# Performance work log

Hardware: AMD Instinct MI355X
Metric: run time of the kernel (lower is better)

The kernel has to match this reference:

```python
import jax, jax.numpy as jnp
import numpy as np

N_NODES = 50000
N_EDGES = 600000
N_GRAPHS = 256
D = 128          # hidden_dim
L = 4            # num_layer
OUT = 1          # output_dim
ATOM_DIMS = [119, 5, 12, 12, 10, 6, 6, 2, 2]   # table size = dim+1, pad to 120
BOND_DIMS = [6, 6, 2, 2, 2]                    # table size = dim+1, pad to 7
BN_EPS = 1e-5


def setup_inputs() -> dict:
    key = jax.random.key(0)
    ks = jax.random.split(key, 16)
    x = jax.random.randint(ks[0], (N_NODES, 9), 0, 3)
    edge_index = jax.random.randint(ks[1], (2, N_EDGES), 0, N_NODES)
    edge_attr = jax.random.randint(ks[2], (N_EDGES, 5), 0, 3)
    batch = jnp.sort(jax.random.randint(ks[3], (N_NODES,), 0, N_GRAPHS))
    s = 0.1
    # padded atom embedding tables: [9, 120, D] (rows beyond dim+1 unused)
    atom_emb = jax.random.normal(ks[4], (9, 120, D), jnp.float32) * s
    # padded bond tables per layer: [L, 5, 7, D]
    bond_emb = jax.random.normal(ks[5], (L, 5, 7, D), jnp.float32) * s
    lin_w = jax.random.normal(ks[6], (L, D, D), jnp.float32) * (1.0 / np.sqrt(D))
    lin_b = jnp.zeros((L, D), jnp.float32)
    bn_gamma = jnp.ones((L, D), jnp.float32)
    bn_beta = jnp.zeros((L, D), jnp.float32)
    mlp_w1 = jax.random.normal(ks[7], (D // 2, D), jnp.float32) * (1.0 / np.sqrt(D))
    mlp_b1 = jnp.zeros((D // 2,), jnp.float32)
    mlp_w2 = jax.random.normal(ks[8], (OUT, D // 2), jnp.float32) * (1.0 / np.sqrt(D // 2))
    mlp_b2 = jnp.zeros((OUT,), jnp.float32)
    return dict(x=x, edge_index=edge_index, edge_attr=edge_attr, batch=batch,
                atom_emb=atom_emb, bond_emb=bond_emb, lin_w=lin_w, lin_b=lin_b,
                bn_gamma=bn_gamma, bn_beta=bn_beta,
                mlp_w1=mlp_w1, mlp_b1=mlp_b1, mlp_w2=mlp_w2, mlp_b2=mlp_b2)


def _multi_embed(tables, idx):
    # tables: [F, V, D], idx: [N, F] -> sum_f tables[f][idx[:, f]]
    return jax.vmap(lambda t, i: t[i], in_axes=(0, 1))(tables, idx).sum(0)


def reference(x, edge_index, edge_attr, batch, atom_emb, bond_emb, lin_w, lin_b,
              bn_gamma, bn_beta, mlp_w1, mlp_b1, mlp_w2, mlp_b2):
    n = x.shape[0]
    loop = jnp.arange(n, dtype=edge_index.dtype)
    src = jnp.concatenate([edge_index[0], loop])           # x_j (source)
    dst = jnp.concatenate([edge_index[1], loop])           # aggregate into target i
    ea = jnp.concatenate([edge_attr, jnp.zeros((n, 5), edge_attr.dtype)], axis=0)
    h = _multi_embed(atom_emb, x)                          # [N, D]
    for l in range(L):
        e_emb = _multi_embed(bond_emb[l], ea)              # [E+N, D]
        msg = h[src] + e_emb                               # gather + add
        aggr = jax.ops.segment_sum(msg, dst, num_segments=n)
        z = aggr @ lin_w[l].T + lin_b[l]
        mu = z.mean(0)
        var = z.var(0)                                     # biased, matches torch BN fwd
        h = jax.nn.relu((z - mu) * jax.lax.rsqrt(var + BN_EPS) * bn_gamma[l] + bn_beta[l])
    # global mean pool
    sums = jax.ops.segment_sum(h, batch, num_segments=N_GRAPHS)
    cnt = jax.ops.segment_sum(jnp.ones((n,), h.dtype), batch, num_segments=N_GRAPHS)
    g = sums / jnp.maximum(cnt, 1.0)[:, None]
    # MLP head (dropout inactive at inference)
    out = jax.nn.relu(g @ mlp_w1.T + mlp_b1) @ mlp_w2.T + mlp_b2
    return out
```

## Files before the change

kernel.cpp:

```cpp
#include <hip/hip_runtime.h>
#include <hip/hip_bf16.h>
#include <stdint.h>

#define D 128
#define NGRAPH 256
#define BN_EPS 1e-5f
#define TAB_ROWS 105
#define TAB_SZ (TAB_ROWS * D)
#define AGG_BLOCKS 512
#define AGG_THREADS 1024
#define MAXDEG 48
#define GW_TS 136

typedef unsigned short u16;
typedef __attribute__((ext_vector_type(8))) short bf16x8;
typedef __attribute__((ext_vector_type(4))) float f32x4;

__device__ inline u16 f2bf(float a) {
  return __builtin_bit_cast(u16, __float2bfloat16(a));
}
__device__ inline uint32_t pk2(float a, float b) {
  return (uint32_t)f2bf(a) | ((uint32_t)f2bf(b) << 16);
}
__device__ inline float bflo(uint32_t u) { return __builtin_bit_cast(float, u << 16); }
__device__ inline float bfhi(uint32_t u) { return __builtin_bit_cast(float, u & 0xffff0000u); }
__device__ inline void unpack8(uint4 v, float* f) {
  f[0] = bflo(v.x); f[1] = bfhi(v.x); f[2] = bflo(v.y); f[3] = bfhi(v.y);
  f[4] = bflo(v.z); f[5] = bfhi(v.z); f[6] = bflo(v.w); f[7] = bfhi(v.w);
}

__global__ __launch_bounds__(256) void setup_kernel(
    const int* __restrict__ x, const float* __restrict__ atom_emb,
    float* __restrict__ h0,
    const int* __restrict__ src, const int* __restrict__ dst,
    const int* __restrict__ attr, int* __restrict__ deg,
    uint2* __restrict__ edges, int ne,
    const int* __restrict__ batch, int* __restrict__ goff,
    float* __restrict__ gsum, int n) {
  int b = blockIdx.x, tid = threadIdx.x;
  int nscat = (ne + 255) >> 8;
  int nemb = (n * 32 + 255) >> 8;
  if (b < nscat) {
    int e = b * 256 + tid;
    if (e >= ne) return;
    int d = dst[e];
    int slot = atomicAdd(&deg[d], 1);
    if (slot >= MAXDEG) return;
    int a0 = attr[e * 5 + 0], a1 = attr[e * 5 + 1], a2 = attr[e * 5 + 2];
    int a3 = attr[e * 5 + 3], a4 = attr[e * 5 + 4];
    uint32_t packed = (uint32_t)(a0 * 7 + a1) | ((uint32_t)(a2 * 7 + a3) << 8) |
                      ((uint32_t)a4 << 16);
    uint2 r; r.x = (uint32_t)src[e]; r.y = packed;
    edges[(size_t)d * MAXDEG + slot] = r;
  } else if (b < nscat + nemb) {
    int t = (b - nscat) * 256 + tid;
    int node = t >> 5, cq = t & 31;
    if (node >= n) return;
    float4 acc = {0.f, 0.f, 0.f, 0.f};
#pragma unroll
    for (int f = 0; f < 9; f++) {
      int idx = x[node * 9 + f];
      const float4* row = (const float4*)(atom_emb + ((size_t)f * 120 + idx) * D);
      float4 v = row[cq];
      acc.x += v.x; acc.y += v.y; acc.z += v.z; acc.w += v.w;
    }
    ((float4*)(h0 + (size_t)node * D))[cq] = acc;
  } else {
    if (b == nscat + nemb) {
      for (int t = tid; t < 4 * 2 * D; t += 256) gsum[t] = 0.f;
    }
    int i = (b - nscat - nemb) * 256 + tid;
    if (i >= n) return;
    int bb = batch[i];
    if (i == 0) {
      for (int g = 0; g <= bb; g++) goff[g] = 0;
    } else {
      int pb = batch[i - 1];
      for (int g = pb + 1; g <= bb; g++) goff[g] = i;
    }
    if (i == n - 1) {
      for (int g = bb + 1; g <= NGRAPH; g++) goff[g] = n;
    }
  }
}

__global__ __launch_bounds__(128) void prep_kernel(
    const float* __restrict__ bemb, const float* __restrict__ linw,
    u16* __restrict__ tabAll) {
  __shared__ float row[D];
  int b = blockIdx.x, c = threadIdx.x;
  int l = b / TAB_ROWS, r = b % TAB_ROWS;
  const float* bond = bemb + (size_t)l * 5 * 7 * D;
  const float* W = linw + (size_t)l * D * D;
  float v;
  if (r < 49)
    v = bond[(0 * 7 + r / 7) * D + c] + bond[(1 * 7 + r % 7) * D + c];
  else if (r < 98) {
    int rr = r - 49;
    v = bond[(2 * 7 + rr / 7) * D + c] + bond[(3 * 7 + rr % 7) * D + c];
  } else
    v = bond[(4 * 7 + (r - 98)) * D + c];
  row[c] = v;
  __syncthreads();
  float s = 0.f;
  for (int k = 0; k < D; k++) s += row[k] * W[(size_t)c * D + k];
  tabAll[((size_t)l * TAB_ROWS + r) * D + c] = f2bf(s);
}

__global__ __launch_bounds__(256) void gemm_kernel(const float* __restrict__ in,
                                                   const float* __restrict__ W,
                                                   const float* __restrict__ gsum,
                                                   const float* __restrict__ gamma,
                                                   const float* __restrict__ beta,
                                                   float invN,
                                                   u16* __restrict__ out, int M) {
  __shared__ u16 wlds[128 * GW_TS];
  __shared__ float bns[2 * D];
  int tid = threadIdx.x;
  for (int i = tid; i < 4096; i += 256) {
    int row = i >> 5, c4 = (i & 31) * 4;
    float4 v = ((const float4*)W)[i];
    uint2 o = {pk2(v.x, v.y), pk2(v.z, v.w)};
    *(uint2*)(wlds + row * GW_TS + c4) = o;
  }
  if (gsum && tid < D) {
    float s = gsum[tid], q = gsum[D + tid];
    float mu = s * invN;
    float var = q * invN - mu * mu;
    float sc = rsqrtf(var + BN_EPS) * gamma[tid];
    bns[tid] = sc;
    bns[D + tid] = beta[tid] - mu * sc;
  }
  __syncthreads();

  int wave = tid >> 6, lane = tid & 63;
  int quad = lane >> 4, l16 = lane & 15;
  int m0 = blockIdx.x * 64 + wave * 16;
  int m = m0 + l16;
  bool valid = m < M;

  f32x4 acc[8];
#pragma unroll
  for (int t = 0; t < 8; t++) acc[t] = (f32x4){0.f, 0.f, 0.f, 0.f};

#pragma unroll
  for (int kk = 0; kk < 4; kk++) {
    int k0 = kk * 32 + quad * 8;
    bf16x8 a;
    if (valid) {
      float4 v0 = *(const float4*)(in + (size_t)m * D + k0);
      float4 v1 = *(const float4*)(in + (size_t)m * D + k0 + 4);
      if (gsum) {
        float4 sc0 = *(const float4*)(bns + k0);
        float4 sc1 = *(const float4*)(bns + k0 + 4);
        float4 sh0 = *(const float4*)(bns + D + k0);
        float4 sh1 = *(const float4*)(bns + D + k0 + 4);
        v0.x = fmaxf(v0.x * sc0.x + sh0.x, 0.f);
        v0.y = fmaxf(v0.y * sc0.y + sh0.y, 0.f);
        v0.z = fmaxf(v0.z * sc0.z + sh0.z, 0.f);
        v0.w = fmaxf(v0.w * sc0.w + sh0.w, 0.f);
        v1.x = fmaxf(v1.x * sc1.x + sh1.x, 0.f);
        v1.y = fmaxf(v1.y * sc1.y + sh1.y, 0.f);
        v1.z = fmaxf(v1.z * sc1.z + sh1.z, 0.f);
        v1.w = fmaxf(v1.w * sc1.w + sh1.w, 0.f);
      }
      uint4 pa = {pk2(v0.x, v0.y), pk2(v0.z, v0.w), pk2(v1.x, v1.y), pk2(v1.z, v1.w)};
      a = __builtin_bit_cast(bf16x8, pa);
    } else {
      uint4 pz = {0u, 0u, 0u, 0u};
      a = __builtin_bit_cast(bf16x8, pz);
    }
#pragma unroll
    for (int nt = 0; nt < 8; nt++) {
      int nrow = nt * 16 + l16;
      uint4 braw = *(const uint4*)(wlds + nrow * GW_TS + k0);
      bf16x8 bfrag = __builtin_bit_cast(bf16x8, braw);
      acc[nt] = __builtin_amdgcn_mfma_f32_16x16x32_bf16(a, bfrag, acc[nt], 0, 0, 0);
    }
  }
#pragma unroll
  for (int r = 0; r < 4; r++) {
    int row = m0 + quad * 4 + r;
    if (row < M) {
#pragma unroll
      for (int nt = 0; nt < 8; nt++)
        out[(size_t)row * D + nt * 16 + l16] = f2bf(acc[nt][r]);
    }
  }
}

__global__ __launch_bounds__(AGG_THREADS) void agg_kernel(
    const u16* __restrict__ ht, const u16* __restrict__ tabT,
    const float* __restrict__ linb, const uint2* __restrict__ edges,
    const int* __restrict__ deg, float* __restrict__ z,
    float* __restrict__ gsum, int n) {
  __shared__ u16 tabs[TAB_SZ];
  __shared__ float psum[2 * D];
  int tid = threadIdx.x;
  for (int i = tid; i < TAB_SZ / 8; i += AGG_THREADS)
    ((uint4*)tabs)[i] = ((const uint4*)tabT)[i];
  if (tid < 2 * D) psum[tid] = 0.f;
  __syncthreads();

  int lane = tid & 63;
  int g = lane >> 4;
  int c8 = lane & 15;
  int wid = (blockIdx.x * AGG_THREADS + tid) >> 6;
  int nw = (gridDim.x * AGG_THREADS) >> 6;

  float lb[8], zb[8];
  {
    float4 l0 = ((const float4*)linb)[c8 * 2];
    float4 l1 = ((const float4*)linb)[c8 * 2 + 1];
    lb[0] = l0.x; lb[1] = l0.y; lb[2] = l0.z; lb[3] = l0.w;
    lb[4] = l1.x; lb[5] = l1.y; lb[6] = l1.z; lb[7] = l1.w;
    float t0[8], t1[8], t2[8];
    unpack8(*(const uint4*)(tabs + 0 * D + c8 * 8), t0);
    unpack8(*(const uint4*)(tabs + 49 * D + c8 * 8), t1);
    unpack8(*(const uint4*)(tabs + 98 * D + c8 * 8), t2);
#pragma unroll
    for (int i = 0; i < 8; i++) zb[i] = t0[i] + t1[i] + t2[i];
  }
  float ssum[8], ssq[8];
#pragma unroll
  for (int i = 0; i < 8; i++) { ssum[i] = 0.f; ssq[i] = 0.f; }

  for (int node = wid; node < n; node += nw) {
    float acc[8];
    if (g == 0) {
      float sv[8];
      unpack8(*(const uint4*)(ht + (size_t)node * D + c8 * 8), sv);
#pragma unroll
      for (int i = 0; i < 8; i++) acc[i] = sv[i] + lb[i] + zb[i];
    } else {
#pragma unroll
      for (int i = 0; i < 8; i++) acc[i] = 0.f;
    }
    int cnt = deg[node]; cnt = (cnt > MAXDEG) ? MAXDEG : cnt;
    int base = node * MAXDEG, e = base + cnt;
    for (int j = base + g; j < e; j += 4) {
      uint2 rec = edges[j];
      uint4 hvv = *(const uint4*)(ht + (size_t)rec.x * D + c8 * 8);
      uint32_t p = rec.y;
      uint4 t0v = *(const uint4*)(tabs + (p & 255u) * D + c8 * 8);
      uint4 t1v = *(const uint4*)(tabs + (49u + ((p >> 8) & 255u)) * D + c8 * 8);
      uint4 t2v = *(const uint4*)(tabs + (98u + (p >> 16)) * D + c8 * 8);
      float hv[8], b0[8], b1[8], b2[8];
      unpack8(hvv, hv); unpack8(t0v, b0); unpack8(t1v, b1); unpack8(t2v, b2);
#pragma unroll
      for (int i = 0; i < 8; i++) acc[i] += hv[i] + b0[i] + b1[i] + b2[i];
    }
#pragma unroll
    for (int off = 16; off <= 32; off <<= 1)
#pragma unroll
      for (int i = 0; i < 8; i++) acc[i] += __shfl_xor(acc[i], off, 64);
    if (g == 0) {
      float4 za = {acc[0], acc[1], acc[2], acc[3]};
      float4 zb4 = {acc[4], acc[5], acc[6], acc[7]};
      float4* zr = (float4*)(z + (size_t)node * D);
      zr[c8 * 2] = za;
      zr[c8 * 2 + 1] = zb4;
#pragma unroll
      for (int i = 0; i < 8; i++) {
        ssum[i] += acc[i];
        ssq[i] += acc[i] * acc[i];
      }
    }
  }
  if (g == 0) {
    int c0 = c8 * 8;
#pragma unroll
    for (int i = 0; i < 8; i++) {
      atomicAdd(&psum[c0 + i], ssum[i]);
      atomicAdd(&psum[D + c0 + i], ssq[i]);
    }
  }
  __syncthreads();
  if (tid < 2 * D) atomicAdd(&gsum[tid], psum[tid]);
}

__global__ __launch_bounds__(512) void poolmlp_kernel(
    const float* __restrict__ z, const float* __restrict__ gsum,
    const float* __restrict__ gamma, const float* __restrict__ beta,
    float invN, const int* __restrict__ goff,
    const float* __restrict__ w1, const float* __restrict__ b1,
    const float* __restrict__ w2, const float* __restrict__ b2,
    float* __restrict__ out) {
  __shared__ float sdata[512];
  __shared__ float pg[D];
  int g = blockIdx.x;
  int c = threadIdx.x & 127, r4 = threadIdx.x >> 7;
  float s0 = gsum[c], q0 = gsum[D + c];
  float mu = s0 * invN;
  float var = q0 * invN - mu * mu;
  float sc = rsqrtf(var + BN_EPS) * gamma[c];
  float sh = beta[c] - mu * sc;
  int s = goff[g], cnt = goff[g + 1] - s;
  float acc = 0.f;
  for (int i = r4; i < cnt; i += 4) {
    float zv = z[(size_t)(s + i) * D + c];
    acc += fmaxf(zv * sc + sh, 0.f);
  }
  sdata[threadIdx.x] = acc;
  __syncthreads();
  if (r4 == 0) {
    float t = sdata[c] + sdata[128 + c] + sdata[256 + c] + sdata[384 + c];
    pg[c] = t / fmaxf((float)cnt, 1.f);
  }
  __syncthreads();
  if (threadIdx.x < 64) {
    int j = threadIdx.x;
    float v = b1[j];
    for (int k = 0; k < D; k++) v += pg[k] * w1[(size_t)j * D + k];
    v = fmaxf(v, 0.f) * w2[j];
#pragma unroll
    for (int off = 32; off > 0; off >>= 1) v += __shfl_down(v, off, 64);
    if (j == 0) out[g] = v + b2[0];
  }
}

extern "C" void kernel_launch(void* const* d_in, const int* in_sizes, int n_in,
                              void* d_out, int out_size, void* d_ws, size_t ws_size,
                              hipStream_t stream) {
  const int*   x     = (const int*)d_in[0];
  const int*   eidx  = (const int*)d_in[1];
  const int*   eattr = (const int*)d_in[2];
  const int*   batch = (const int*)d_in[3];
  const float* aemb  = (const float*)d_in[4];
  const float* bemb  = (const float*)d_in[5];
  const float* linw  = (const float*)d_in[6];
  const float* linb  = (const float*)d_in[7];
  const float* gamma = (const float*)d_in[8];
  const float* beta  = (const float*)d_in[9];
  const float* w1    = (const float*)d_in[10];
  const float* b1    = (const float*)d_in[11];
  const float* w2    = (const float*)d_in[12];
  const float* b2    = (const float*)d_in[13];
  float* out = (float*)d_out;

  int n  = in_sizes[3];
  int ne = in_sizes[1] / 2;
  float invN = 1.f / (float)n;

  char* p = (char*)d_ws;
  auto alloc = [&](size_t bytes) {
    char* r = p;
    p += (bytes + 255) & ~(size_t)255;
    return r;
  };
  float* bufA   = (float*)alloc((size_t)n * D * 4);
  u16*   bufB   = (u16*)alloc((size_t)n * D * 2);
  uint2* edges  = (uint2*)alloc((size_t)n * MAXDEG * 8);
  int*   deg    = (int*)alloc((size_t)n * 4);
  int*   goff   = (int*)alloc((size_t)(NGRAPH + 1) * 4);
  u16*   tabAll = (u16*)alloc((size_t)4 * TAB_SZ * 2);
  float* gsum   = (float*)alloc((size_t)4 * 2 * D * 4);

  hipMemsetAsync(deg, 0, (size_t)n * 4, stream);

  int nscat = (ne + 255) >> 8;
  int nemb = (n * 32 + 255) >> 8;
  int ngoff = (n + 255) >> 8;
  setup_kernel<<<nscat + nemb + ngoff, 256, 0, stream>>>(
      x, aemb, bufA, eidx, eidx + ne, eattr, deg, edges, ne, batch, goff,
      gsum, n);
  prep_kernel<<<4 * TAB_ROWS, 128, 0, stream>>>(bemb, linw, tabAll);

  for (int l = 0; l < 4; l++) {
    gemm_kernel<<<(n + 63) / 64, 256, 0, stream>>>(
        bufA, linw + (size_t)l * D * D,
        l ? (gsum + (size_t)(l - 1) * 2 * D) : (const float*)nullptr,
        l ? (gamma + (size_t)(l - 1) * D) : (const float*)nullptr,
        l ? (beta + (size_t)(l - 1) * D) : (const float*)nullptr,
        invN, bufB, n);
    agg_kernel<<<AGG_BLOCKS, AGG_THREADS, 0, stream>>>(
        bufB, tabAll + (size_t)l * TAB_SZ, linb + (size_t)l * D, edges, deg,
        bufA, gsum + (size_t)l * 2 * D, n);
  }
  poolmlp_kernel<<<NGRAPH, 512, 0, stream>>>(
      bufA, gsum + 3 * 2 * D, gamma + 3 * D, beta + 3 * D, invN, goff,
      w1, b1, w2, b2, out);
}
```

Measured before the change: 436.7 us.

## Prefetch edge gathers in aggregation, pre-convert swizzled bf16 weights, widen GEMM tiles

The aggregation kernel now loads up to six edge records and their neighbour rows before accumulating, and prefetches the next node's degree, so more gathers are in flight per wave. It also moves from 512 blocks of 1024 threads to 2048 blocks of 256. The prep kernel converts the linear weights to bf16 once, with an XOR swizzle that avoids LDS bank conflicts, so each GEMM block does a plain copy instead of converting and padding per block. Each GEMM wave now computes 32 rows and reuses every B fragment for two MFMAs, which halves the number of blocks. These changes raise register pressure and add a second code path for edges beyond the prefetch depth.

```diff
diff --git a/kernel.cpp b/kernel.cpp
--- a/kernel.cpp
+++ b/kernel.cpp
@@ -7,10 +7,11 @@
 #define BN_EPS 1e-5f
 #define TAB_ROWS 105
 #define TAB_SZ (TAB_ROWS * D)
-#define AGG_BLOCKS 512
-#define AGG_THREADS 1024
+#define AGG_BLOCKS 2048
+#define AGG_THREADS 256
 #define MAXDEG 48
-#define GW_TS 136
+#define PF 6
+#define GEMM_ROWS 128
 
 typedef unsigned short u16;
 typedef __attribute__((ext_vector_type(8))) short bf16x8;
@@ -86,43 +87,46 @@
 
 __global__ __launch_bounds__(128) void prep_kernel(
     const float* __restrict__ bemb, const float* __restrict__ linw,
-    u16* __restrict__ tabAll) {
+    u16* __restrict__ tabAll, u16* __restrict__ wball) {
   __shared__ float row[D];
   int b = blockIdx.x, c = threadIdx.x;
-  int l = b / TAB_ROWS, r = b % TAB_ROWS;
-  const float* bond = bemb + (size_t)l * 5 * 7 * D;
-  const float* W = linw + (size_t)l * D * D;
-  float v;
-  if (r < 49)
-    v = bond[(0 * 7 + r / 7) * D + c] + bond[(1 * 7 + r % 7) * D + c];
-  else if (r < 98) {
-    int rr = r - 49;
-    v = bond[(2 * 7 + rr / 7) * D + c] + bond[(3 * 7 + rr % 7) * D + c];
-  } else
-    v = bond[(4 * 7 + (r - 98)) * D + c];
-  row[c] = v;
-  __syncthreads();
-  float s = 0.f;
-  for (int k = 0; k < D; k++) s += row[k] * W[(size_t)c * D + k];
-  tabAll[((size_t)l * TAB_ROWS + r) * D + c] = f2bf(s);
+  if (b < 4 * TAB_ROWS) {
+    int l = b / TAB_ROWS, r = b % TAB_ROWS;
+    const float* bond = bemb + (size_t)l * 5 * 7 * D;
+    const float* W = linw + (size_t)l * D * D;
+    float v;
+    if (r < 49)
+      v = bond[(0 * 7 + r / 7) * D + c] + bond[(1 * 7 + r % 7) * D + c];
+    else if (r < 98) {
+      int rr = r - 49;
+      v = bond[(2 * 7 + rr / 7) * D + c] + bond[(3 * 7 + rr % 7) * D + c];
+    } else
+      v = bond[(4 * 7 + (r - 98)) * D + c];
+    row[c] = v;
+    __syncthreads();
+    float s = 0.f;
+    for (int k = 0; k < D; k++) s += row[k] * W[(size_t)c * D + k];
+    tabAll[((size_t)l * TAB_ROWS + r) * D + c] = f2bf(s);
+  } else {
+    int i = b - 4 * TAB_ROWS;
+    int l = i >> 7, j = i & 127;
+    float v = linw[(size_t)l * D * D + (size_t)j * D + c];
+    wball[(size_t)l * D * D + (size_t)j * D + (c ^ ((j & 7) << 3))] = f2bf(v);
+  }
 }
 
 __global__ __launch_bounds__(256) void gemm_kernel(const float* __restrict__ in,
-                                                   const float* __restrict__ W,
+                                                   const u16* __restrict__ Wb,
                                                    const float* __restrict__ gsum,
                                                    const float* __restrict__ gamma,
                                                    const float* __restrict__ beta,
                                                    float invN,
                                                    u16* __restrict__ out, int M) {
-  __shared__ u16 wlds[128 * GW_TS];
+  __shared__ u16 wlds[D * D];
   __shared__ float bns[2 * D];
   int tid = threadIdx.x;
-  for (int i = tid; i < 4096; i += 256) {
-    int row = i >> 5, c4 = (i & 31) * 4;
-    float4 v = ((const float4*)W)[i];
-    uint2 o = {pk2(v.x, v.y), pk2(v.z, v.w)};
-    *(uint2*)(wlds + row * GW_TS + c4) = o;
-  }
+  for (int i = tid; i < D * D / 8; i += 256)
+    ((uint4*)wlds)[i] = ((const uint4*)Wb)[i];
   if (gsum && tid < D) {
     float s = gsum[tid], q = gsum[D + tid];
     float mu = s * invN;
@@ -135,58 +139,65 @@
 
   int wave = tid >> 6, lane = tid & 63;
   int quad = lane >> 4, l16 = lane & 15;
-  int m0 = blockIdx.x * 64 + wave * 16;
-  int m = m0 + l16;
-  bool valid = m < M;
-
-  f32x4 acc[8];
-#pragma unroll
-  for (int t = 0; t < 8; t++) acc[t] = (f32x4){0.f, 0.f, 0.f, 0.f};
+  int m0 = blockIdx.x * GEMM_ROWS + wave * 32;
+
+  f32x4 acc[2][8];
+#pragma unroll
+  for (int mt = 0; mt < 2; mt++)
+#pragma unroll
+    for (int t = 0; t < 8; t++) acc[mt][t] = (f32x4){0.f, 0.f, 0.f, 0.f};
 
 #pragma unroll
   for (int kk = 0; kk < 4; kk++) {
     int k0 = kk * 32 + quad * 8;
-    bf16x8 a;
-    if (valid) {
-      float4 v0 = *(const float4*)(in + (size_t)m * D + k0);
-      float4 v1 = *(const float4*)(in + (size_t)m * D + k0 + 4);
-      if (gsum) {
-        float4 sc0 = *(const float4*)(bns + k0);
-        float4 sc1 = *(const float4*)(bns + k0 + 4);
-        float4 sh0 = *(const float4*)(bns + D + k0);
-        float4 sh1 = *(const float4*)(bns + D + k0 + 4);
-        v0.x = fmaxf(v0.x * sc0.x + sh0.x, 0.f);
-        v0.y = fmaxf(v0.y * sc0.y + sh0.y, 0.f);
-        v0.z = fmaxf(v0.z * sc0.z + sh0.z, 0.f);
-        v0.w = fmaxf(v0.w * sc0.w + sh0.w, 0.f);
-        v1.x = fmaxf(v1.x * sc1.x + sh1.x, 0.f);
-        v1.y = fmaxf(v1.y * sc1.y + sh1.y, 0.f);
-        v1.z = fmaxf(v1.z * sc1.z + sh1.z, 0.f);
-        v1.w = fmaxf(v1.w * sc1.w + sh1.w, 0.f);
+    bf16x8 a[2];
+#pragma unroll
+    for (int mt = 0; mt < 2; mt++) {
+      int m = m0 + mt * 16 + l16;
+      if (m < M) {
+        float4 v0 = *(const float4*)(in + (size_t)m * D + k0);
+        float4 v1 = *(const float4*)(in + (size_t)m * D + k0 + 4);
+        if (gsum) {
+          float4 sc0 = *(const float4*)(bns + k0);
+          float4 sc1 = *(const float4*)(bns + k0 + 4);
+          float4 sh0 = *(const float4*)(bns + D + k0);
+          float4 sh1 = *(const float4*)(bns + D + k0 + 4);
+          v0.x = fmaxf(v0.x * sc0.x + sh0.x, 0.f);
+          v0.y = fmaxf(v0.y * sc0.y + sh0.y, 0.f);
+          v0.z = fmaxf(v0.z * sc0.z + sh0.z, 0.f);
+          v0.w = fmaxf(v0.w * sc0.w + sh0.w, 0.f);
+          v1.x = fmaxf(v1.x * sc1.x + sh1.x, 0.f);
+          v1.y = fmaxf(v1.y * sc1.y + sh1.y, 0.f);
+          v1.z = fmaxf(v1.z * sc1.z + sh1.z, 0.f);
+          v1.w = fmaxf(v1.w * sc1.w + sh1.w, 0.f);
+        }
+        uint4 pa = {pk2(v0.x, v0.y), pk2(v0.z, v0.w), pk2(v1.x, v1.y), pk2(v1.z, v1.w)};
+        a[mt] = __builtin_bit_cast(bf16x8, pa);
+      } else {
+        uint4 pz = {0u, 0u, 0u, 0u};
+        a[mt] = __builtin_bit_cast(bf16x8, pz);
       }
-      uint4 pa = {pk2(v0.x, v0.y), pk2(v0.z, v0.w), pk2(v1.x, v1.y), pk2(v1.z, v1.w)};
-      a = __builtin_bit_cast(bf16x8, pa);
-    } else {
-      uint4 pz = {0u, 0u, 0u, 0u};
-      a = __builtin_bit_cast(bf16x8, pz);
     }
 #pragma unroll
     for (int nt = 0; nt < 8; nt++) {
       int nrow = nt * 16 + l16;
-      uint4 braw = *(const uint4*)(wlds + nrow * GW_TS + k0);
+      uint4 braw = *(const uint4*)(wlds + nrow * D + (k0 ^ ((nrow & 7) << 3)));
       bf16x8 bfrag = __builtin_bit_cast(bf16x8, braw);
-      acc[nt] = __builtin_amdgcn_mfma_f32_16x16x32_bf16(a, bfrag, acc[nt], 0, 0, 0);
-    }
-  }
-#pragma unroll
-  for (int r = 0; r < 4; r++) {
-    int row = m0 + quad * 4 + r;
-    if (row < M) {
-#pragma unroll
-      for (int nt = 0; nt < 8; nt++)
-        out[(size_t)row * D + nt * 16 + l16] = f2bf(acc[nt][r]);
-    }
-  }
+      acc[0][nt] = __builtin_amdgcn_mfma_f32_16x16x32_bf16(a[0], bfrag, acc[0][nt], 0, 0, 0);
+      acc[1][nt] = __builtin_amdgcn_mfma_f32_16x16x32_bf16(a[1], bfrag, acc[1][nt], 0, 0, 0);
+    }
+  }
+#pragma unroll
+  for (int mt = 0; mt < 2; mt++)
+#pragma unroll
+    for (int r = 0; r < 4; r++) {
+      int row = m0 + mt * 16 + quad * 4 + r;
+      if (row < M) {
+#pragma unroll
+        for (int nt = 0; nt < 8; nt++)
+          out[(size_t)row * D + nt * 16 + l16] = f2bf(acc[mt][nt][r]);
+      }
+    }
 }
 
 __global__ __launch_bounds__(AGG_THREADS) void agg_kernel(
@@ -225,7 +236,20 @@
 #pragma unroll
   for (int i = 0; i < 8; i++) { ssum[i] = 0.f; ssq[i] = 0.f; }
 
+  int dg = (wid < n) ? deg[wid] : 0;
   for (int node = wid; node < n; node += nw) {
+    int cnt = (dg > MAXDEG) ? MAXDEG : dg;
+    int nxt = node + nw;
+    if (nxt < n) dg = deg[nxt];
+    int base = node * MAXDEG;
+    int e = base + cnt;
+    int j0 = base + g;
+
+    uint2 rec[PF];
+#pragma unroll
+    for (int t = 0; t < PF; t++)
+      if (j0 + t * 4 < e) rec[t] = edges[j0 + t * 4];
+
     float acc[8];
     if (g == 0) {
       float sv[8];
@@ -236,20 +260,39 @@
 #pragma unroll
       for (int i = 0; i < 8; i++) acc[i] = 0.f;
     }
-    int cnt = deg[node]; cnt = (cnt > MAXDEG) ? MAXDEG : cnt;
-    int base = node * MAXDEG, e = base + cnt;
-    for (int j = base + g; j < e; j += 4) {
-      uint2 rec = edges[j];
-      uint4 hvv = *(const uint4*)(ht + (size_t)rec.x * D + c8 * 8);
-      uint32_t p = rec.y;
+
+    uint4 hvv[PF];
+#pragma unroll
+    for (int t = 0; t < PF; t++)
+      if (j0 + t * 4 < e)
+        hvv[t] = *(const uint4*)(ht + (size_t)rec[t].x * D + c8 * 8);
+
+#pragma unroll
+    for (int t = 0; t < PF; t++) {
+      if (j0 + t * 4 < e) {
+        uint32_t p = rec[t].y;
+        uint4 t0v = *(const uint4*)(tabs + (p & 255u) * D + c8 * 8);
+        uint4 t1v = *(const uint4*)(tabs + (49u + ((p >> 8) & 255u)) * D + c8 * 8);
+        uint4 t2v = *(const uint4*)(tabs + (98u + (p >> 16)) * D + c8 * 8);
+        float hv[8], b0[8], b1[8], b2[8];
+        unpack8(hvv[t], hv); unpack8(t0v, b0); unpack8(t1v, b1); unpack8(t2v, b2);
+#pragma unroll
+        for (int i = 0; i < 8; i++) acc[i] += hv[i] + b0[i] + b1[i] + b2[i];
+      }
+    }
+    for (int j = j0 + PF * 4; j < e; j += 4) {
+      uint2 r2 = edges[j];
+      uint4 hv4 = *(const uint4*)(ht + (size_t)r2.x * D + c8 * 8);
+      uint32_t p = r2.y;
       uint4 t0v = *(const uint4*)(tabs + (p & 255u) * D + c8 * 8);
       uint4 t1v = *(const uint4*)(tabs + (49u + ((p >> 8) & 255u)) * D + c8 * 8);
       uint4 t2v = *(const uint4*)(tabs + (98u + (p >> 16)) * D + c8 * 8);
       float hv[8], b0[8], b1[8], b2[8];
-      unpack8(hvv, hv); unpack8(t0v, b0); unpack8(t1v, b1); unpack8(t2v, b2);
+      unpack8(hv4, hv); unpack8(t0v, b0); unpack8(t1v, b1); unpack8(t2v, b2);
 #pragma unroll
       for (int i = 0; i < 8; i++) acc[i] += hv[i] + b0[i] + b1[i] + b2[i];
     }
+
 #pragma unroll
     for (int off = 16; off <= 32; off <<= 1)
 #pragma unroll
@@ -354,6 +397,7 @@
   int*   deg    = (int*)alloc((size_t)n * 4);
   int*   goff   = (int*)alloc((size_t)(NGRAPH + 1) * 4);
   u16*   tabAll = (u16*)alloc((size_t)4 * TAB_SZ * 2);
+  u16*   wball  = (u16*)alloc((size_t)4 * D * D * 2);
   float* gsum   = (float*)alloc((size_t)4 * 2 * D * 4);
 
   hipMemsetAsync(deg, 0, (size_t)n * 4, stream);
@@ -364,11 +408,11 @@
   setup_kernel<<<nscat + nemb + ngoff, 256, 0, stream>>>(
       x, aemb, bufA, eidx, eidx + ne, eattr, deg, edges, ne, batch, goff,
       gsum, n);
-  prep_kernel<<<4 * TAB_ROWS, 128, 0, stream>>>(bemb, linw, tabAll);
+  prep_kernel<<<4 * TAB_ROWS + 4 * D, 128, 0, stream>>>(bemb, linw, tabAll, wball);
 
   for (int l = 0; l < 4; l++) {
-    gemm_kernel<<<(n + 63) / 64, 256, 0, stream>>>(
-        bufA, linw + (size_t)l * D * D,
+    gemm_kernel<<<(n + GEMM_ROWS - 1) / GEMM_ROWS, 256, 0, stream>>>(
+        bufA, wball + (size_t)l * D * D,
         l ? (gsum + (size_t)(l - 1) * 2 * D) : (const float*)nullptr,
         l ? (gamma + (size_t)(l - 1) * D) : (const float*)nullptr,
         l ? (beta + (size_t)(l - 1) * D) : (const float*)nullptr,
```

After: 545.9 us. +25.0%, slower.
